# Kernel tuning notes

Hardware: AMD Instinct MI355X
Metric: run time of the kernel (lower is better)

Reference implementation:

```python
import jax, jax.numpy as jnp
import numpy as np

N_NODES = 100000
N_EDGES = 1_600_000
IN_CH = 64
HID = 128
OUT_CH = 2


def _glorot(key, shape):
    fan_in = shape[0]
    return jax.random.normal(key, shape, dtype=jnp.float32) / jnp.sqrt(jnp.float32(fan_in))


def setup_inputs() -> dict:
    key = jax.random.key(0)
    ks = jax.random.split(key, 10)
    x = jax.random.normal(ks[0], (N_NODES, IN_CH), dtype=jnp.float32)
    edge_index = jax.random.randint(ks[1], (2, N_EDGES), 0, N_NODES, dtype=jnp.int64)
    # SAGEConv layer 0: lin_l (neighbor, with bias) + lin_r (root)
    W_n0 = _glorot(ks[2], (IN_CH, HID))
    W_s0 = _glorot(ks[3], (IN_CH, HID))
    b0 = jnp.zeros((HID,), dtype=jnp.float32)
    # SAGEConv layer 1
    W_n1 = _glorot(ks[4], (HID, HID))
    W_s1 = _glorot(ks[5], (HID, HID))
    b1 = jnp.zeros((HID,), dtype=jnp.float32)
    # final fc
    fc_w = _glorot(ks[6], (HID, OUT_CH))
    fc_b = jnp.zeros((OUT_CH,), dtype=jnp.float32)
    return {"x": x, "edge_index": edge_index, "W_n0": W_n0, "W_s0": W_s0, "b0": b0,
            "W_n1": W_n1, "W_s1": W_s1, "b1": b1, "fc_w": fc_w, "fc_b": fc_b}


def _sage_conv(h, src, dst, W_n, W_s, b, num_nodes):
    # mean aggregation of source features onto destination nodes
    agg = jax.ops.segment_sum(h[src], dst, num_segments=num_nodes)  # [N, d]
    cnt = jax.ops.segment_sum(jnp.ones_like(dst, dtype=h.dtype), dst, num_segments=num_nodes)
    mean = agg / jnp.maximum(cnt, 1.0)[:, None]
    return mean @ W_n + h @ W_s + b


def reference(x, edge_index, W_n0, W_s0, b0, W_n1, W_s1, b1, fc_w, fc_b):
    src, dst = edge_index[0], edge_index[1]
    n = x.shape[0]
    h = jax.nn.relu(_sage_conv(x, src, dst, W_n0, W_s0, b0, n))  # dropout is identity in eval mode
    h = jax.nn.relu(_sage_conv(h, src, dst, W_n1, W_s1, b1, n))
    return h @ fc_w + fc_b
```

## Files before the change

kernel.cpp:

```cpp
#include <hip/hip_runtime.h>

#define N_NODES 100000
#define IN_CH 64
#define HID 128
#define BSH 8
#define NBUCK ((N_NODES + 255) >> 8)
#define NCB 512

typedef short short8 __attribute__((ext_vector_type(8)));
typedef float floatx4 __attribute__((ext_vector_type(4)));
typedef float floatx2 __attribute__((ext_vector_type(2)));

__device__ __forceinline__ unsigned short f2bf(float f) {
    unsigned u = __builtin_bit_cast(unsigned, f);
    u += 0x7fffu + ((u >> 16) & 1u);
    return (unsigned short)(u >> 16);
}

template <int K>
__device__ __forceinline__ void pack_dev(const float* __restrict__ Wn,
                                         const float* __restrict__ Ws,
                                         unsigned short* __restrict__ Bpack, int idx) {
    int s = idx >> 9;
    int rem = idx & 511;
    int t = rem >> 6;
    int lane = rem & 63;
    int quad = lane >> 4;
    int n = t * 16 + (lane & 15);
    unsigned short v[8];
#pragma unroll
    for (int j = 0; j < 8; ++j) {
        int k = s * 32 + quad * 8 + j;
        float w = (k < K) ? Wn[(size_t)k * HID + n] : Ws[(size_t)(k - K) * HID + n];
        v[j] = f2bf(w);
    }
    *(short8*)(Bpack + (size_t)idx * 8) = *(short8*)v;
}

__global__ __launch_bounds__(256) void histprep_kernel(const int* __restrict__ dst,
                                                       int* __restrict__ table, int E, int chunk,
                                                       const float* __restrict__ x,
                                                       unsigned short* __restrict__ x_bf,
                                                       unsigned char* __restrict__ x_f8,
                                                       const float* __restrict__ Wn0,
                                                       const float* __restrict__ Ws0,
                                                       unsigned short* __restrict__ Bpack0,
                                                       const float* __restrict__ Wn1,
                                                       const float* __restrict__ Ws1,
                                                       unsigned short* __restrict__ Bpack1,
                                                       int* __restrict__ scan_done, int n4) {
    int b = blockIdx.x;
    if (b < NCB) {
        if (b == 0 && threadIdx.x == 0) *scan_done = 0;
        __shared__ int h[NBUCK];
        for (int i = threadIdx.x; i < NBUCK; i += 256) h[i] = 0;
        __syncthreads();
        int e0 = b * chunk;
        int e1 = min(E, e0 + chunk);
        for (int e = e0 + threadIdx.x; e < e1; e += 256) atomicAdd(&h[dst[e] >> BSH], 1);
        __syncthreads();
        for (int i = threadIdx.x; i < NBUCK; i += 256) table[i * NCB + b] = h[i];
    } else if (b < NCB + 8) {
        pack_dev<IN_CH>(Wn0, Ws0, Bpack0, (b - NCB) * 256 + threadIdx.x);
    } else if (b < NCB + 24) {
        pack_dev<HID>(Wn1, Ws1, Bpack1, (b - NCB - 8) * 256 + threadIdx.x);
    } else {
        int i = (b - NCB - 24) * 256 + threadIdx.x;
        if (i < n4) {
            float4 v = ((const float4*)x)[i];
            ushort4 o;
            o.x = f2bf(v.x); o.y = f2bf(v.y); o.z = f2bf(v.z); o.w = f2bf(v.w);
            ((ushort4*)x_bf)[i] = o;
            int p8 = __builtin_amdgcn_cvt_pk_fp8_f32(v.x, v.y, 0, false);
            p8 = __builtin_amdgcn_cvt_pk_fp8_f32(v.z, v.w, p8, true);
            ((unsigned*)x_f8)[i] = (unsigned)p8;
        }
    }
}

__global__ __launch_bounds__(256) void scan12_kernel(int* __restrict__ table,
                                                     int* __restrict__ tot,
                                                     int* __restrict__ bstart,
                                                     int* __restrict__ ptr,
                                                     int* __restrict__ scan_done, int E) {
    __shared__ int s[256];
    __shared__ int lastflag;
    int b = blockIdx.x, t = threadIdx.x;
    int c0 = table[b * NCB + 2 * t];
    int c1 = table[b * NCB + 2 * t + 1];
    int s2 = c0 + c1;
    s[t] = s2;
    __syncthreads();
#pragma unroll
    for (int off = 1; off < 256; off <<= 1) {
        int v = (t >= off) ? s[t - off] : 0;
        __syncthreads();
        s[t] += v;
        __syncthreads();
    }
    int excl2 = s[t] - s2;
    table[b * NCB + 2 * t] = excl2;
    table[b * NCB + 2 * t + 1] = excl2 + c0;
    if (t == 255) {
        __hip_atomic_store(&tot[b], s[255], __ATOMIC_RELAXED, __HIP_MEMORY_SCOPE_AGENT);
        int prev = __hip_atomic_fetch_add(scan_done, 1, __ATOMIC_ACQ_REL, __HIP_MEMORY_SCOPE_AGENT);
        lastflag = (prev == NBUCK - 1);
    }
    __syncthreads();
    if (!lastflag) return;
    int v0 = (2 * t < NBUCK)
                 ? __hip_atomic_load(&tot[2 * t], __ATOMIC_RELAXED, __HIP_MEMORY_SCOPE_AGENT) : 0;
    int v1 = (2 * t + 1 < NBUCK)
                 ? __hip_atomic_load(&tot[2 * t + 1], __ATOMIC_RELAXED, __HIP_MEMORY_SCOPE_AGENT) : 0;
    int p2 = v0 + v1;
    __syncthreads();
    s[t] = p2;
    __syncthreads();
#pragma unroll
    for (int off = 1; off < 256; off <<= 1) {
        int u = (t >= off) ? s[t - off] : 0;
        __syncthreads();
        s[t] += u;
        __syncthreads();
    }
    int e2 = s[t] - p2;
    if (2 * t < NBUCK) bstart[2 * t] = e2;
    if (2 * t + 1 < NBUCK) bstart[2 * t + 1] = e2 + v0;
    if (t == 0) {
        bstart[NBUCK] = E;
        ptr[N_NODES] = E;
    }
}

__global__ __launch_bounds__(256) void bin_kernel(const int* __restrict__ src,
                                                  const int* __restrict__ dst,
                                                  const int* __restrict__ table,
                                                  const int* __restrict__ bstart,
                                                  unsigned* __restrict__ binned, int E, int chunk) {
    __shared__ int cur[NBUCK];
    int blk = blockIdx.x;
    for (int i = threadIdx.x; i < NBUCK; i += 256) cur[i] = bstart[i] + table[i * NCB + blk];
    __syncthreads();
    int e0 = blk * chunk;
    int e1 = min(E, e0 + chunk);
    for (int e = e0 + threadIdx.x; e < e1; e += 256) {
        int d = dst[e];
        int b = d >> BSH;
        int pos = atomicAdd(&cur[b], 1);
        if ((unsigned)pos < (unsigned)E)
            binned[pos] = (unsigned)src[e] | ((unsigned)(d & 255) << 17);
    }
}

__global__ __launch_bounds__(256) void place_kernel(const unsigned* __restrict__ binned,
                                                    const int* __restrict__ bstart,
                                                    int* __restrict__ ptr,
                                                    int* __restrict__ sorted, int N, int E) {
    __shared__ int deg[256];
    __shared__ int cur[256];
    __shared__ int ssum[256];
    int b = blockIdx.x, t = threadIdx.x;
    int start = bstart[b], end = bstart[b + 1];
    start = max(0, min(start, E));
    end = max(start, min(end, E));
    deg[t] = 0;
    __syncthreads();
    for (int i = start + t; i < end; i += 256) atomicAdd(&deg[(binned[i] >> 17) & 255], 1);
    __syncthreads();
    int a = deg[t];
    ssum[t] = a;
    __syncthreads();
#pragma unroll
    for (int off = 1; off < 256; off <<= 1) {
        int u = (t >= off) ? ssum[t - off] : 0;
        __syncthreads();
        ssum[t] += u;
        __syncthreads();
    }
    int excl = ssum[t] - a;
    cur[t] = excl;
    int n0 = b * 256 + t;
    if (n0 < N) ptr[n0] = start + excl;
    __syncthreads();
    for (int i = start + t; i < end; i += 256) {
        unsigned p = binned[i];
        int dl = (p >> 17) & 255;
        int pos = start + atomicAdd(&cur[dl], 1);
        if ((unsigned)pos < (unsigned)E) sorted[pos] = (int)(p & 0x1FFFF);
    }
}

template <int C>
__global__ __launch_bounds__(256) void gather_mean_w16(const int* __restrict__ ptr,
                                                       const int* __restrict__ srcs,
                                                       const unsigned char* __restrict__ feat,
                                                       unsigned short* __restrict__ mean, int N,
                                                       int E) {
    constexpr int R = C / 16;
    constexpr int LOGR = (C == 64) ? 2 : 3;
    constexpr int NPW = 64 / R;
    const int lane = threadIdx.x & 63;
    const int g = lane >> LOGR;
    const int l = lane & (R - 1);
    const int w = (blockIdx.x * 4 + (threadIdx.x >> 6)) * NPW + g;
    if (w >= N) return;
    int s0 = ptr[w], s1 = ptr[w + 1];
    s0 = max(0, min(s0, E));
    s1 = max(s0, min(s1, E));
    const int deg = min(s1 - s0, 4096);

    floatx2 accq[4][8];
#pragma unroll
    for (int q = 0; q < 4; ++q)
#pragma unroll
        for (int u = 0; u < 8; ++u) { accq[q][u][0] = 0.0f; accq[q][u][1] = 0.0f; }

    const int nfull = deg & ~3;
    int j = 0;
    if (nfull > 0) {
        int cid[4];
#pragma unroll
        for (int q = 0; q < 4; ++q)
            cid[q] = (int)min((unsigned)srcs[s0 + q], (unsigned)(N_NODES - 1));
        for (; j < nfull; j += 4) {
            uint4 v[4];
#pragma unroll
            for (int q = 0; q < 4; ++q)
                v[q] = *(const uint4*)(feat + (size_t)cid[q] * C + l * 16);
            int base = (j + 4 < nfull) ? s0 + j + 4 : s0;
            int cidn[4];
#pragma unroll
            for (int q = 0; q < 4; ++q)
                cidn[q] = (int)min((unsigned)srcs[base + q], (unsigned)(N_NODES - 1));
#pragma unroll
            for (int q = 0; q < 4; ++q) {
                const uint dw[4] = {v[q].x, v[q].y, v[q].z, v[q].w};
#pragma unroll
                for (int d = 0; d < 4; ++d) {
                    accq[q][2 * d + 0] += __builtin_amdgcn_cvt_pk_f32_fp8(dw[d], false);
                    accq[q][2 * d + 1] += __builtin_amdgcn_cvt_pk_f32_fp8(dw[d], true);
                }
            }
#pragma unroll
            for (int q = 0; q < 4; ++q) cid[q] = cidn[q];
        }
    }
    if (j < deg) {
        int cid[4];
#pragma unroll
        for (int q = 0; q < 4; ++q) {
            int jj = min(j + q, deg - 1);
            cid[q] = (int)min((unsigned)srcs[s0 + jj], (unsigned)(N_NODES - 1));
        }
        uint4 v[4];
#pragma unroll
        for (int q = 0; q < 4; ++q)
            v[q] = *(const uint4*)(feat + (size_t)cid[q] * C + l * 16);
#pragma unroll
        for (int q = 0; q < 4; ++q) {
            uint dw[4] = {v[q].x, v[q].y, v[q].z, v[q].w};
#pragma unroll
            for (int d = 0; d < 4; ++d) dw[d] = (j + q < deg) ? dw[d] : 0u;
#pragma unroll
            for (int d = 0; d < 4; ++d) {
                accq[q][2 * d + 0] += __builtin_amdgcn_cvt_pk_f32_fp8(dw[d], false);
                accq[q][2 * d + 1] += __builtin_amdgcn_cvt_pk_f32_fp8(dw[d], true);
            }
        }
    }
#pragma unroll
    for (int u = 0; u < 8; ++u) {
        accq[0][u] += accq[1][u];
        accq[2][u] += accq[3][u];
        accq[0][u] += accq[2][u];
    }
    const float inv = (deg > 0) ? 1.0f / (float)deg : 0.0f;
    unsigned short o[16];
#pragma unroll
    for (int u = 0; u < 8; ++u) {
        o[2 * u + 0] = f2bf(accq[0][u][0] * inv);
        o[2 * u + 1] = f2bf(accq[0][u][1] * inv);
    }
    unsigned short* mp = mean + (size_t)w * C + l * 16;
    *(uint4*)(mp + 0) = ((const uint4*)o)[0];
    *(uint4*)(mp + 8) = ((const uint4*)o)[1];
}

template <int KT, bool FUSE_FC>
__global__ __launch_bounds__(256) void sage_gemm_mfma(const unsigned short* __restrict__ meanb,
                                                      const unsigned short* __restrict__ hb,
                                                      const unsigned short* __restrict__ Bpack,
                                                      const float* __restrict__ bias,
                                                      const float* __restrict__ fcw,
                                                      const float* __restrict__ fcb,
                                                      unsigned short* __restrict__ outb,
                                                      unsigned char* __restrict__ out8,
                                                      float* __restrict__ outf, int N) {
    constexpr int KH = KT / 2;
    constexpr int LDA = KT + 8;
    __shared__ unsigned short As[64 * LDA];
    const int t = threadIdx.x;
    const int row0 = blockIdx.x * 64;

    constexpr int SEGS = KT / 8;
    for (int c = t; c < 64 * SEGS; c += 256) {
        int r = c / SEGS, seg = c % SEGS;
        int rsrc = row0 + r;
        if (rsrc >= N) rsrc = N - 1;
        const unsigned short* srcp = (seg < SEGS / 2)
                                         ? meanb + (size_t)rsrc * KH + seg * 8
                                         : hb + (size_t)rsrc * KH + (seg - SEGS / 2) * 8;
        *(uint4*)&As[r * LDA + seg * 8] = *(const uint4*)srcp;
    }
    __syncthreads();

    const int lane = t & 63;
    const int wave = t >> 6;
    const int quad = lane >> 4;
    const int lo = lane & 15;

    floatx4 acc[8];
#pragma unroll
    for (int i = 0; i < 8; ++i)
#pragma unroll
        for (int r = 0; r < 4; ++r) acc[i][r] = 0.0f;

    const unsigned short* abase = &As[(wave * 16 + lo) * LDA + quad * 8];
#pragma unroll
    for (int s = 0; s < KT / 32; ++s) {
        short8 a = *(const short8*)(abase + s * 32);
        const short8* bp = (const short8*)Bpack + (size_t)(s * 8) * 64 + lane;
#pragma unroll
        for (int tt = 0; tt < 8; ++tt) {
            short8 b = bp[tt * 64];
            acc[tt] = __builtin_amdgcn_mfma_f32_16x16x32_bf16(a, b, acc[tt], 0, 0, 0);
        }
    }

    if (!FUSE_FC) {
        __syncthreads();
#pragma unroll
        for (int tt = 0; tt < 8; ++tt) {
            int col = tt * 16 + lo;
            float bv = bias[col];
#pragma unroll
            for (int r = 0; r < 4; ++r) {
                int rl = wave * 16 + quad * 4 + r;
                As[rl * LDA + col] = f2bf(fmaxf(acc[tt][r] + bv, 0.0f));
            }
        }
        __syncthreads();
        for (int i = t; i < 64 * (HID / 8); i += 256) {
            int r = i >> 4, ch = i & 15;
            int row = row0 + r;
            if (row < N)
                *(uint4*)(outb + (size_t)row * HID + ch * 8) = *(const uint4*)&As[r * LDA + ch * 8];
        }
        __syncthreads();
        unsigned char* As8 = (unsigned char*)As;
#pragma unroll
        for (int tt = 0; tt < 8; ++tt) {
            int col = tt * 16 + lo;
            float bv = bias[col];
#pragma unroll
            for (int r = 0; r < 4; ++r) {
                int rl = wave * 16 + quad * 4 + r;
                float v = fmaxf(acc[tt][r] + bv, 0.0f);
                int p8 = __builtin_amdgcn_cvt_pk_fp8_f32(v, v, 0, false);
                As8[rl * (LDA * 2) + col] = (unsigned char)(p8 & 0xff);
            }
        }
        __syncthreads();
        for (int i = t; i < 64 * (HID / 16); i += 256) {
            int r = i >> 3, ch = i & 7;
            int row = row0 + r;
            if (row < N)
                *(uint4*)(out8 + (size_t)row * HID + ch * 16) =
                    *(const uint4*)&As8[r * (LDA * 2) + ch * 16];
        }
    } else {
        float o0[4] = {}, o1[4] = {};
#pragma unroll
        for (int tt = 0; tt < 8; ++tt) {
            int col = tt * 16 + lo;
            float bv = bias[col];
            float w0 = fcw[col * 2 + 0];
            float w1 = fcw[col * 2 + 1];
#pragma unroll
            for (int r = 0; r < 4; ++r) {
                float v = fmaxf(acc[tt][r] + bv, 0.0f);
                o0[r] += v * w0;
                o1[r] += v * w1;
            }
        }
#pragma unroll
        for (int r = 0; r < 4; ++r) {
#pragma unroll
            for (int m = 8; m >= 1; m >>= 1) {
                o0[r] += __shfl_xor(o0[r], m, 16);
                o1[r] += __shfl_xor(o1[r], m, 16);
            }
        }
        if (lo == 0) {
#pragma unroll
            for (int r = 0; r < 4; ++r) {
                int row = row0 + wave * 16 + quad * 4 + r;
                if (row < N) {
                    outf[(size_t)row * 2 + 0] = o0[r] + fcb[0];
                    outf[(size_t)row * 2 + 1] = o1[r] + fcb[1];
                }
            }
        }
    }
}

extern "C" void kernel_launch(void* const* d_in, const int* in_sizes, int n_in,
                              void* d_out, int out_size, void* d_ws, size_t ws_size,
                              hipStream_t stream) {
    const float* x   = (const float*)d_in[0];
    const int*   ei  = (const int*)d_in[1];
    const float* Wn0 = (const float*)d_in[2];
    const float* Ws0 = (const float*)d_in[3];
    const float* b0  = (const float*)d_in[4];
    const float* Wn1 = (const float*)d_in[5];
    const float* Ws1 = (const float*)d_in[6];
    const float* b1  = (const float*)d_in[7];
    const float* fcw = (const float*)d_in[8];
    const float* fcb = (const float*)d_in[9];
    float* out = (float*)d_out;

    const int E = in_sizes[1] / 2;
    const int* src = ei;
    const int* dst = ei + E;
    const int N = N_NODES;
    const int chunk = (E + NCB - 1) / NCB;

    char* ws = (char*)d_ws;
    size_t off = 0;
    int* table  = (int*)(ws + off); off += (size_t)NBUCK * NCB * 4;
    int* tot    = (int*)(ws + off); off += 4096;
    int* bstart = (int*)(ws + off); off += 4096;
    int* scan_done = (int*)(ws + off); off += 256;
    int* ptr    = (int*)(ws + off); off += (size_t)(N + 1) * 4 + 60; off &= ~(size_t)63;
    unsigned* binned = (unsigned*)(ws + off); off += (size_t)E * 4;
    int* sorted = (int*)(ws + off); off += (size_t)E * 4;
    off = (off + 255) & ~(size_t)255;
    unsigned short* x_bf   = (unsigned short*)(ws + off); off += (size_t)N * IN_CH * 2;
    unsigned short* mean0  = (unsigned short*)(ws + off); off += (size_t)N * IN_CH * 2;
    unsigned short* h1_bf  = (unsigned short*)(ws + off); off += (size_t)N * HID * 2;
    unsigned short* mean1  = (unsigned short*)(ws + off); off += (size_t)N * HID * 2;
    unsigned char*  h1_f8  = (unsigned char*)(ws + off);  off += (size_t)N * HID;
    unsigned char*  x_f8   = (unsigned char*)(ws + off);  off += (size_t)N * IN_CH;
    off = (off + 255) & ~(size_t)255;
    unsigned short* Bpack0 = (unsigned short*)(ws + off); off += (size_t)(2 * IN_CH / 32) * 8 * 64 * 8 * 2;
    unsigned short* Bpack1 = (unsigned short*)(ws + off); off += (size_t)(2 * HID / 32) * 8 * 64 * 8 * 2;

    {
        int n4 = N * IN_CH / 4;
        int nblk = NCB + 24 + (n4 + 255) / 256;
        histprep_kernel<<<nblk, 256, 0, stream>>>(dst, table, E, chunk, x, x_bf, x_f8,
                                                  Wn0, Ws0, Bpack0, Wn1, Ws1, Bpack1,
                                                  scan_done, n4);
    }
    scan12_kernel<<<NBUCK, 256, 0, stream>>>(table, tot, bstart, ptr, scan_done, E);
    bin_kernel<<<NCB, 256, 0, stream>>>(src, dst, table, bstart, binned, E, chunk);
    place_kernel<<<NBUCK, 256, 0, stream>>>(binned, bstart, ptr, sorted, N, E);

    gather_mean_w16<IN_CH><<<(N + 63) / 64, 256, 0, stream>>>(ptr, sorted, x_f8, mean0, N, E);
    sage_gemm_mfma<2 * IN_CH, false><<<(N + 63) / 64, 256, 0, stream>>>(
        mean0, x_bf, Bpack0, b0, nullptr, nullptr, h1_bf, h1_f8, nullptr, N);

    gather_mean_w16<HID><<<(N + 31) / 32, 256, 0, stream>>>(ptr, sorted, h1_f8, mean1, N, E);
    sage_gemm_mfma<2 * HID, true><<<(N + 63) / 64, 256, 0, stream>>>(
        mean1, h1_bf, Bpack1, b1, fcw, fcb, nullptr, nullptr, out, N);
}
```

Before: 236.2 us.

## Sort nodes by in-degree so gather wavefront groups have balanced work

```diff
diff --git a/kernel.cpp b/kernel.cpp
--- a/kernel.cpp
+++ b/kernel.cpp
@@ -48,10 +48,15 @@
                                                        const float* __restrict__ Wn1,
                                                        const float* __restrict__ Ws1,
                                                        unsigned short* __restrict__ Bpack1,
-                                                       int* __restrict__ scan_done, int n4) {
+                                                       int* __restrict__ scan_done,
+                                                       int* __restrict__ dhist,
+                                                       int* __restrict__ cursor, int n4) {
     int b = blockIdx.x;
     if (b < NCB) {
-        if (b == 0 && threadIdx.x == 0) *scan_done = 0;
+        if (b == 0) {
+            if (threadIdx.x == 0) *scan_done = 0;
+            if (threadIdx.x < 64) { dhist[threadIdx.x] = 0; cursor[threadIdx.x] = 0; }
+        }
         __shared__ int h[NBUCK];
         for (int i = threadIdx.x; i < NBUCK; i += 256) h[i] = 0;
         __syncthreads();
@@ -155,20 +160,25 @@
 __global__ __launch_bounds__(256) void place_kernel(const unsigned* __restrict__ binned,
                                                     const int* __restrict__ bstart,
                                                     int* __restrict__ ptr,
-                                                    int* __restrict__ sorted, int N, int E) {
+                                                    int* __restrict__ sorted,
+                                                    int* __restrict__ dhist, int N, int E) {
     __shared__ int deg[256];
     __shared__ int cur[256];
     __shared__ int ssum[256];
+    __shared__ int h64[64];
     int b = blockIdx.x, t = threadIdx.x;
     int start = bstart[b], end = bstart[b + 1];
     start = max(0, min(start, E));
     end = max(start, min(end, E));
     deg[t] = 0;
+    if (t < 64) h64[t] = 0;
     __syncthreads();
     for (int i = start + t; i < end; i += 256) atomicAdd(&deg[(binned[i] >> 17) & 255], 1);
     __syncthreads();
     int a = deg[t];
     ssum[t] = a;
+    int n0 = b * 256 + t;
+    if (n0 < N) atomicAdd(&h64[min(a, 63)], 1);
     __syncthreads();
 #pragma unroll
     for (int off = 1; off < 256; off <<= 1) {
@@ -179,8 +189,8 @@
     }
     int excl = ssum[t] - a;
     cur[t] = excl;
-    int n0 = b * 256 + t;
     if (n0 < N) ptr[n0] = start + excl;
+    if (t < 64 && h64[t] > 0) atomicAdd(&dhist[t], h64[t]);
     __syncthreads();
     for (int i = start + t; i < end; i += 256) {
         unsigned p = binned[i];
@@ -190,8 +200,45 @@
     }
 }
 
+__global__ __launch_bounds__(256) void nperm_kernel(const int* __restrict__ ptr,
+                                                    const int* __restrict__ dhist,
+                                                    int* __restrict__ cursor,
+                                                    int* __restrict__ nperm, int N) {
+    __shared__ int h[64];
+    __shared__ int r[64];
+    __shared__ int base[64];
+    const int b = blockIdx.x, t = threadIdx.x;
+    const int n = b * 256 + t;
+    int d = 0;
+    if (n < N) {
+        int s0 = ptr[n], s1 = ptr[n + 1];
+        d = min(max(s1 - s0, 0), 63);
+    }
+    if (t < 64) h[t] = 0;
+    __syncthreads();
+    if (n < N) atomicAdd(&h[d], 1);
+    __syncthreads();
+    if (t < 64) {
+        r[t] = (h[t] > 0) ? atomicAdd(&cursor[t], h[t]) : 0;
+        base[t] = dhist[t];
+    }
+    __syncthreads();
+    if (t == 0) {
+        int acc = 0;
+#pragma unroll
+        for (int i = 0; i < 64; ++i) { int v = base[i]; base[i] = acc; acc += v; }
+    }
+    if (t < 64) h[t] = 0;
+    __syncthreads();
+    if (n < N) {
+        int pos = base[d] + r[d] + atomicAdd(&h[d], 1);
+        if ((unsigned)pos < (unsigned)N) nperm[pos] = n;
+    }
+}
+
 template <int C>
-__global__ __launch_bounds__(256) void gather_mean_w16(const int* __restrict__ ptr,
+__global__ __launch_bounds__(256) void gather_mean_w16(const int* __restrict__ nperm,
+                                                       const int* __restrict__ ptr,
                                                        const int* __restrict__ srcs,
                                                        const unsigned char* __restrict__ feat,
                                                        unsigned short* __restrict__ mean, int N,
@@ -202,8 +249,10 @@
     const int lane = threadIdx.x & 63;
     const int g = lane >> LOGR;
     const int l = lane & (R - 1);
-    const int w = (blockIdx.x * 4 + (threadIdx.x >> 6)) * NPW + g;
-    if (w >= N) return;
+    const int idx = (blockIdx.x * 4 + (threadIdx.x >> 6)) * NPW + g;
+    if (idx >= N) return;
+    int w = nperm[idx];
+    w = (int)min((unsigned)w, (unsigned)(N - 1));
     int s0 = ptr[w], s1 = ptr[w + 1];
     s0 = max(0, min(s0, E));
     s1 = max(s0, min(s1, E));
@@ -441,6 +490,9 @@
     int* tot    = (int*)(ws + off); off += 4096;
     int* bstart = (int*)(ws + off); off += 4096;
     int* scan_done = (int*)(ws + off); off += 256;
+    int* dhist  = (int*)(ws + off); off += 256;
+    int* cursor = (int*)(ws + off); off += 256;
+    int* nperm  = (int*)(ws + off); off += (size_t)N * 4;
     int* ptr    = (int*)(ws + off); off += (size_t)(N + 1) * 4 + 60; off &= ~(size_t)63;
     unsigned* binned = (unsigned*)(ws + off); off += (size_t)E * 4;
     int* sorted = (int*)(ws + off); off += (size_t)E * 4;
@@ -460,17 +512,18 @@
         int nblk = NCB + 24 + (n4 + 255) / 256;
         histprep_kernel<<<nblk, 256, 0, stream>>>(dst, table, E, chunk, x, x_bf, x_f8,
                                                   Wn0, Ws0, Bpack0, Wn1, Ws1, Bpack1,
-                                                  scan_done, n4);
+                                                  scan_done, dhist, cursor, n4);
     }
     scan12_kernel<<<NBUCK, 256, 0, stream>>>(table, tot, bstart, ptr, scan_done, E);
     bin_kernel<<<NCB, 256, 0, stream>>>(src, dst, table, bstart, binned, E, chunk);
-    place_kernel<<<NBUCK, 256, 0, stream>>>(binned, bstart, ptr, sorted, N, E);
-
-    gather_mean_w16<IN_CH><<<(N + 63) / 64, 256, 0, stream>>>(ptr, sorted, x_f8, mean0, N, E);
+    place_kernel<<<NBUCK, 256, 0, stream>>>(binned, bstart, ptr, sorted, dhist, N, E);
+    nperm_kernel<<<(N + 255) / 256, 256, 0, stream>>>(ptr, dhist, cursor, nperm, N);
+
+    gather_mean_w16<IN_CH><<<(N + 63) / 64, 256, 0, stream>>>(nperm, ptr, sorted, x_f8, mean0, N, E);
     sage_gemm_mfma<2 * IN_CH, false><<<(N + 63) / 64, 256, 0, stream>>>(
         mean0, x_bf, Bpack0, b0, nullptr, nullptr, h1_bf, h1_f8, nullptr, N);
 
-    gather_mean_w16<HID><<<(N + 31) / 32, 256, 0, stream>>>(ptr, sorted, h1_f8, mean1, N, E);
+    gather_mean_w16<HID><<<(N + 31) / 32, 256, 0, stream>>>(nperm, ptr, sorted, h1_f8, mean1, N, E);
     sage_gemm_mfma<2 * HID, true><<<(N + 63) / 64, 256, 0, stream>>>(
         mean1, h1_bf, Bpack1, b1, fcw, fcb, nullptr, nullptr, out, N);
 }
```

After: 251.8 us. 1.07x slower.
